# Kernel optimization log

Measured on AMD Instinct MI355X. Metric: run time of the kernel, lower is better.

## Reference

```python
import jax, jax.numpy as jnp
import numpy as np

B, S, IN, H, E, OUT = 64, 2048, 256, 512, 256, 32000


def setup_inputs() -> dict:
    key = jax.random.key(0)
    ks = jax.random.split(key, 20)
    g = lambda k, shp, fan_in: jax.random.normal(k, shp, jnp.float32) / jnp.sqrt(jnp.float32(fan_in))
    return {
        "x": jax.random.normal(ks[0], (B, IN), jnp.float32),
        "hidden": jax.random.normal(ks[1], (B, H), jnp.float32),
        "encoder_outputs": jax.random.normal(ks[2], (B, S, H), jnp.float32),
        # attention params
        "W1_w": g(ks[3], (H, E), H), "W1_b": jnp.zeros((E,), jnp.float32),
        "W2_w": g(ks[4], (H, E), H),
        "v_w": g(ks[5], (E, 1), E),
        # GRU gate params (input to gates is concat(x, context): IN+H)
        "Wxr_w": g(ks[6], (IN + H, H), IN + H), "Wxr_b": jnp.zeros((H,), jnp.float32),
        "Whr_w": g(ks[7], (H, H), H),
        "Wxz_w": g(ks[8], (IN + H, H), IN + H), "Wxz_b": jnp.zeros((H,), jnp.float32),
        "Whz_w": g(ks[9], (H, H), H),
        "Wxh_w": g(ks[10], (IN + H, H), IN + H), "Wxh_b": jnp.zeros((H,), jnp.float32),
        "Whh_w": g(ks[11], (H, H), H),
        # output projection
        "Who_w": g(ks[12], (H, OUT), H), "Who_b": jnp.zeros((OUT,), jnp.float32),
    }


def reference(x, hidden, encoder_outputs,
              W1_w, W1_b, W2_w, v_w,
              Wxr_w, Wxr_b, Whr_w,
              Wxz_w, Wxz_b, Whz_w,
              Wxh_w, Wxh_b, Whh_w,
              Who_w, Who_b):
    # Bahdanau attention
    # energy: [B, S, E]
    energy = jnp.tanh(jnp.einsum("bsh,he->bse", encoder_outputs, W1_w) + W1_b
                      + (hidden @ W2_w)[:, None, :])
    scores = jnp.einsum("bse,eo->bs", energy, v_w)          # [B, S]
    attn_weights = jax.nn.softmax(scores, axis=1)            # [B, S]
    context = jnp.einsum("bs,bsh->bh", attn_weights, encoder_outputs)  # [B, H]

    x_context = jnp.concatenate([x, context], axis=-1)       # [B, IN+H]
    reset_gate = jax.nn.sigmoid(x_context @ Wxr_w + Wxr_b + hidden @ Whr_w)
    update_gate = jax.nn.sigmoid(x_context @ Wxz_w + Wxz_b + hidden @ Whz_w)
    h_tilde = jnp.tanh(x_context @ Wxh_w + Wxh_b + (reset_gate * hidden) @ Whh_w)
    new_hidden = update_gate * hidden + (1.0 - update_gate) * h_tilde
    output = new_hidden @ Who_w + Who_b                      # [B, OUT]
    return (output, new_hidden, attn_weights)
```

## Files before the change

### kernel.cpp

```cpp
#include <hip/hip_runtime.h>

#define BB 64
#define SS 2048
#define INDIM 256
#define HH 512
#define EE 256
#define OUTD 32000

typedef __attribute__((ext_vector_type(8))) short short8;
typedef __attribute__((ext_vector_type(4))) float floatx4;

#define LOG2E 1.4426950408889634f

__device__ __forceinline__ unsigned short f2bf(float f) {
  unsigned u = __float_as_uint(f);
  return (unsigned short)((u + 0x7FFFu + ((u >> 16) & 1u)) >> 16);
}
__device__ __forceinline__ unsigned pk2(float a, float b) {
  return (unsigned)f2bf(a) | ((unsigned)f2bf(b) << 16);
}
__device__ __forceinline__ float bf2f(unsigned short u) {
  return __uint_as_float((unsigned)u << 16);
}
__device__ __forceinline__ float fast_tanh(float x) {
  float e = __builtin_amdgcn_exp2f(x * 2.8853900817779268f);
  return 1.0f - 2.0f * __builtin_amdgcn_rcpf(e + 1.0f);
}
__device__ __forceinline__ float fast_sigmoid(float x) {
  float e = __builtin_amdgcn_exp2f(-x * LOG2E);
  return __builtin_amdgcn_rcpf(1.0f + e);
}

typedef __attribute__((address_space(1))) const void g1void;
typedef __attribute__((address_space(3))) void l3void;
__device__ __forceinline__ void dma16(const void* g, void* l) {
  __builtin_amdgcn_global_load_lds((g1void*)g, (l3void*)l, 16, 0, 0);
}

#define WS_W1T   0
#define WS_HBP   262144
#define WS_CTX   786432
#define WS_NHBF  917504
#define WS_GP    1245184
#define WS_NP    6488064
#define WS_CTXP  9109504
#define WS_SUMP  25886720
#define WS_ENCB  25894912

__global__ __launch_bounds__(256) void k_pre(
    const float* __restrict__ enc, unsigned short* __restrict__ encb,
    const float* __restrict__ W1, unsigned short* __restrict__ W1t,
    const float* __restrict__ hidden, const float* __restrict__ W2,
    const float* __restrict__ W1b, float* __restrict__ hbp) {
  int blk = blockIdx.x, tid = threadIdx.x;
  if (blk < 4096) {
    int r_loc = tid >> 3, c0 = tid & 7;
    int row = blk * 32 + r_loc;
    int rs = row & 7;
    const float* src = enc + (size_t)row * HH;
    unsigned short* dst = encb + (size_t)row * HH;
#pragma unroll
    for (int k = 0; k < 8; ++k) {
      int c = c0 + k * 8;
      float4 f0 = *(const float4*)(src + c * 8);
      float4 f1 = *(const float4*)(src + c * 8 + 4);
      uint4 w;
      w.x = pk2(f0.x, f0.y); w.y = pk2(f0.z, f0.w);
      w.z = pk2(f1.x, f1.y); w.w = pk2(f1.z, f1.w);
      *(uint4*)(dst + (c ^ rs) * 8) = w;
    }
  } else if (blk < 4608) {
    int idx = (blk - 4096) * 256 + tid;
    int k = idx >> 8, e = idx & 255;
    W1t[e * HH + k] = f2bf(W1[idx]);
  } else {
    int u = blk - 4608;
    int b0 = (u & 15) * 4, seg = u >> 4, e = tid;
    int h0 = seg * 64;
    float a0 = 0, a1 = 0, a2 = 0, a3 = 0;
    if (seg == 0) { a0 = a1 = a2 = a3 = W1b[e]; }
#pragma unroll 16
    for (int h = 0; h < 64; ++h) {
      float w = W2[(h0 + h) * EE + e];
      a0 += hidden[(b0 + 0) * HH + h0 + h] * w;
      a1 += hidden[(b0 + 1) * HH + h0 + h] * w;
      a2 += hidden[(b0 + 2) * HH + h0 + h] * w;
      a3 += hidden[(b0 + 3) * HH + h0 + h] * w;
    }
    float* o = hbp + (size_t)seg * BB * EE;
    o[(b0 + 0) * EE + e] = a0; o[(b0 + 1) * EE + e] = a1;
    o[(b0 + 2) * EE + e] = a2; o[(b0 + 3) * EE + e] = a3;
  }
}

__global__ __launch_bounds__(256, 2) void k_scores(
    const unsigned short* __restrict__ encb, const unsigned short* __restrict__ W1t,
    const float* __restrict__ hbp, const float* __restrict__ vw,
    float* __restrict__ attn, float* __restrict__ ctxp, float* __restrict__ sump) {
  __shared__ unsigned short Afull[64 * 512];
  __shared__ float hb_s[EE], v_s[EE];
  __shared__ float red[4 * 64];
  __shared__ float wbuf[64];

  int tid = threadIdx.x;
  int m0 = blockIdx.x * 64;
  int b = blockIdx.x >> 5;
  int sloc = (blockIdx.x & 31) * 64;
  int lane = tid & 63, wn = tid >> 6;
  int l15 = lane & 15, quad = lane >> 4;

#pragma unroll
  for (int rr = 0; rr < 16; ++rr) {
    int r = wn * 16 + rr;
    dma16(encb + (size_t)(m0 + r) * HH + lane * 8, Afull + r * HH);
  }
  {
    float hbv = 0.0f;
#pragma unroll
    for (int s = 0; s < 8; ++s) hbv += hbp[s * BB * EE + b * EE + tid];
    hb_s[tid] = hbv;
    v_s[tid] = vw[tid];
  }
  __syncthreads();

  floatx4 acc[4][4];
#pragma unroll
  for (int i = 0; i < 4; ++i)
#pragma unroll
    for (int j = 0; j < 4; ++j) acc[i][j] = (floatx4)0.0f;

  const unsigned short* bbase = W1t + (size_t)(wn * 64) * HH;
#pragma unroll
  for (int kb = 0; kb < 16; ++kb) {
    short8 a[4];
#pragma unroll
    for (int i = 0; i < 4; ++i) {
      int r = i * 16 + l15;
      int pc = (kb * 4 + quad) ^ (l15 & 7);
      a[i] = *(const short8*)(Afull + r * HH + pc * 8);
    }
#pragma unroll
    for (int j = 0; j < 4; ++j) {
      short8 bfr = *(const short8*)(bbase + (size_t)(j * 16 + l15) * HH + kb * 32 + quad * 8);
#pragma unroll
      for (int i = 0; i < 4; ++i)
        acc[i][j] = __builtin_amdgcn_mfma_f32_16x16x32_bf16(a[i], bfr, acc[i][j], 0, 0, 0);
    }
  }
  __syncthreads();

#pragma unroll
  for (int i = 0; i < 4; ++i)
#pragma unroll
    for (int r = 0; r < 4; ++r) {
      float s = 0.0f;
#pragma unroll
      for (int j = 0; j < 4; ++j) {
        int e = wn * 64 + j * 16 + l15;
        s += fast_tanh(acc[i][j][r] + hb_s[e]) * v_s[e];
      }
#pragma unroll
      for (int off = 1; off < 16; off <<= 1) s += __shfl_xor(s, off, 64);
      if (l15 == 0) red[wn * 64 + i * 16 + quad * 4 + r] = s;
    }
  __syncthreads();
  if (tid < 64) {
    float sc = red[tid] + red[64 + tid] + red[128 + tid] + red[192 + tid];
    float e = __builtin_amdgcn_exp2f(sc * LOG2E);
    wbuf[tid] = e;
    attn[b * SS + sloc + tid] = e;
    float s = e;
#pragma unroll
    for (int off = 1; off < 64; off <<= 1) s += __shfl_xor(s, off, 64);
    if (tid == 0) sump[blockIdx.x] = s;
  }
  __syncthreads();

  float cacc[8];
#pragma unroll
  for (int j = 0; j < 8; ++j) cacc[j] = 0.0f;
#pragma unroll
  for (int rr = 0; rr < 16; ++rr) {
    int r = wn * 16 + rr;
    float w = wbuf[r];
    int pc = lane ^ (r & 7);
    short8 av = *(const short8*)(Afull + r * HH + pc * 8);
#pragma unroll
    for (int j = 0; j < 8; ++j) cacc[j] += w * bf2f((unsigned short)av[j]);
  }
  float4 c0, c1;
  c0.x = cacc[0]; c0.y = cacc[1]; c0.z = cacc[2]; c0.w = cacc[3];
  c1.x = cacc[4]; c1.y = cacc[5]; c1.z = cacc[6]; c1.w = cacc[7];
  float* cp = ctxp + ((size_t)blockIdx.x * 4 + wn) * HH + lane * 8;
  *(float4*)cp = c0;
  *(float4*)(cp + 4) = c1;
}

__global__ __launch_bounds__(256) void k_norm(float* __restrict__ attn,
                                              const float* __restrict__ ctxp,
                                              const float* __restrict__ sump,
                                              float* __restrict__ ctx) {
  int b = blockIdx.x >> 1, half = blockIdx.x & 1, tid = threadIdx.x;
  float s = 0.0f;
#pragma unroll
  for (int t = 0; t < 32; ++t) s += sump[b * 32 + t];
  float inv = 1.0f / s;
  int h = half * 256 + tid;
  float c = 0.0f;
#pragma unroll 16
  for (int t = 0; t < 128; ++t) c += ctxp[(size_t)(b * 128 + t) * HH + h];
  ctx[b * HH + h] = c * inv;
#pragma unroll
  for (int i = 0; i < 4; ++i) attn[b * SS + half * 1024 + i * 256 + tid] *= inv;
}

__device__ __forceinline__ void part_seg(
    const float* __restrict__ Wx, const float* __restrict__ Wh,
    const float* __restrict__ x, const float* __restrict__ ctx,
    const float* __restrict__ hv, int seg, int b0, int h,
    float* __restrict__ outp) {
  const float* wseg;
  const float* a0; const float* a1; const float* a2; const float* a3;
  int vk0 = seg * 64;
  if (seg < 4) {
    wseg = Wx + (size_t)vk0 * HH;
    a0 = x + (b0 + 0) * INDIM + vk0;       a1 = x + (b0 + 1) * INDIM + vk0;
    a2 = x + (b0 + 2) * INDIM + vk0;       a3 = x + (b0 + 3) * INDIM + vk0;
  } else if (seg < 12) {
    wseg = Wx + (size_t)vk0 * HH;
    int off = vk0 - 256;
    a0 = ctx + (b0 + 0) * HH + off;        a1 = ctx + (b0 + 1) * HH + off;
    a2 = ctx + (b0 + 2) * HH + off;        a3 = ctx + (b0 + 3) * HH + off;
  } else {
    int off = vk0 - 768;
    wseg = Wh + (size_t)off * HH;
    a0 = hv + (b0 + 0) * HH + off;         a1 = hv + (b0 + 1) * HH + off;
    a2 = hv + (b0 + 2) * HH + off;         a3 = hv + (b0 + 3) * HH + off;
  }
  float s0 = 0, s1 = 0, s2 = 0, s3 = 0;
#pragma unroll 16
  for (int i = 0; i < 64; ++i) {
    float w = wseg[i * HH + h];
    s0 += a0[i] * w; s1 += a1[i] * w;
    s2 += a2[i] * w; s3 += a3[i] * w;
  }
  outp[(b0 + 0) * HH + h] = s0; outp[(b0 + 1) * HH + h] = s1;
  outp[(b0 + 2) * HH + h] = s2; outp[(b0 + 3) * HH + h] = s3;
}

__global__ __launch_bounds__(512) void k_gpart(
    const float* __restrict__ x, const float* __restrict__ ctx,
    const float* __restrict__ hidden,
    const float* __restrict__ Wxr, const float* __restrict__ Whr,
    const float* __restrict__ Wxz, const float* __restrict__ Whz,
    float* __restrict__ gp) {
  int b0 = blockIdx.x * 4, seg = blockIdx.y, sel = blockIdx.z, h = threadIdx.x;
  const float* Wx = sel ? Wxz : Wxr;
  const float* Wh = sel ? Whz : Whr;
  float* outp = gp + (size_t)(sel * 20 + seg) * BB * HH;
  part_seg(Wx, Wh, x, ctx, hidden, seg, b0, h, outp);
}

__global__ __launch_bounds__(512) void k_npart(
    const float* __restrict__ x, const float* __restrict__ ctx,
    const float* __restrict__ hidden, const float* __restrict__ gp,
    const float* __restrict__ Wxrb,
    const float* __restrict__ Wxh, const float* __restrict__ Whh,
    float* __restrict__ np) {
  __shared__ float rh_s[256];
  int b0 = blockIdx.x * 4, seg = blockIdx.y, h = threadIdx.x;
  int vk0 = seg * 64;
  const float* wseg;
  const float* a0; const float* a1; const float* a2; const float* a3;
  if (seg >= 12) {
    int off = vk0 - 768;
    if (h < 256) {
      int bb = h >> 6, k = off + (h & 63);
      float r = Wxrb[k];
#pragma unroll
      for (int s = 0; s < 20; ++s) r += gp[((size_t)s * BB + b0 + bb) * HH + k];
      rh_s[h] = fast_sigmoid(r) * hidden[(b0 + bb) * HH + k];
    }
    __syncthreads();
    wseg = Whh + (size_t)off * HH;
    a0 = rh_s; a1 = rh_s + 64; a2 = rh_s + 128; a3 = rh_s + 192;
  } else if (seg < 4) {
    wseg = Wxh + (size_t)vk0 * HH;
    a0 = x + (b0 + 0) * INDIM + vk0;       a1 = x + (b0 + 1) * INDIM + vk0;
    a2 = x + (b0 + 2) * INDIM + vk0;       a3 = x + (b0 + 3) * INDIM + vk0;
  } else {
    int off = vk0 - 256;
    wseg = Wxh + (size_t)vk0 * HH;
    a0 = ctx + (b0 + 0) * HH + off;        a1 = ctx + (b0 + 1) * HH + off;
    a2 = ctx + (b0 + 2) * HH + off;        a3 = ctx + (b0 + 3) * HH + off;
  }
  float s0 = 0, s1 = 0, s2 = 0, s3 = 0;
#pragma unroll 16
  for (int i = 0; i < 64; ++i) {
    float w = wseg[i * HH + h];
    s0 += a0[i] * w; s1 += a1[i] * w;
    s2 += a2[i] * w; s3 += a3[i] * w;
  }
  float* outp = np + (size_t)seg * BB * HH;
  outp[(b0 + 0) * HH + h] = s0; outp[(b0 + 1) * HH + h] = s1;
  outp[(b0 + 2) * HH + h] = s2; outp[(b0 + 3) * HH + h] = s3;
}

__global__ __launch_bounds__(256) void k_nred(
    const float* __restrict__ np, const float* __restrict__ gp,
    const float* __restrict__ Wxzb, const float* __restrict__ Wxhb,
    const float* __restrict__ hidden,
    float* __restrict__ nh, unsigned short* __restrict__ nhbf) {
  int b = blockIdx.x >> 1, h = (blockIdx.x & 1) * 256 + threadIdx.x;
  float z = Wxzb[h];
#pragma unroll
  for (int s = 0; s < 20; ++s) z += gp[((size_t)(20 + s) * BB + b) * HH + h];
  z = fast_sigmoid(z);
  float a = Wxhb[h];
#pragma unroll
  for (int s = 0; s < 20; ++s) a += np[((size_t)s * BB + b) * HH + h];
  float ht = fast_tanh(a);
  float val = z * hidden[b * HH + h] + (1.0f - z) * ht;
  nh[b * HH + h] = val;
  nhbf[b * HH + h] = f2bf(val);
}

__global__ __launch_bounds__(256) void k_out2(const unsigned short* __restrict__ nhbf,
                                              const float* __restrict__ Who,
                                              const float* __restrict__ Whob,
                                              float* __restrict__ out) {
  int tid = threadIdx.x;
  int lane = tid & 63, w = tid >> 6;
  int l15 = lane & 15, quad = lane >> 4;
  int n = blockIdx.x * 64 + w * 16 + l15;

  floatx4 acc[4];
#pragma unroll
  for (int i = 0; i < 4; ++i) acc[i] = (floatx4)0.0f;

#pragma unroll
  for (int kc = 0; kc < 16; ++kc) {
    int k0 = kc * 32;
    float bf[8];
    const float* bp = Who + (size_t)(k0 + quad * 8) * OUTD + n;
#pragma unroll
    for (int j = 0; j < 8; ++j) bf[j] = bp[(size_t)j * OUTD];
    union { unsigned u[4]; short8 v; } bu;
#pragma unroll
    for (int j = 0; j < 4; ++j) bu.u[j] = pk2(bf[2 * j], bf[2 * j + 1]);
#pragma unroll
    for (int i = 0; i < 4; ++i) {
      short8 af = *(const short8*)(nhbf + (i * 16 + l15) * HH + k0 + quad * 8);
      acc[i] = __builtin_amdgcn_mfma_f32_16x16x32_bf16(af, bu.v, acc[i], 0, 0, 0);
    }
  }
  float bias = Whob[n];
#pragma unroll
  for (int i = 0; i < 4; ++i)
#pragma unroll
    for (int r = 0; r < 4; ++r) {
      int m = i * 16 + quad * 4 + r;
      out[(size_t)m * OUTD + n] = acc[i][r] + bias;
    }
}

extern "C" void kernel_launch(void* const* d_in, const int* in_sizes, int n_in,
                              void* d_out, int out_size, void* d_ws, size_t ws_size,
                              hipStream_t stream) {
  const float* x    = (const float*)d_in[0];
  const float* hid  = (const float*)d_in[1];
  const float* enc  = (const float*)d_in[2];
  const float* W1w  = (const float*)d_in[3];
  const float* W1b  = (const float*)d_in[4];
  const float* W2w  = (const float*)d_in[5];
  const float* vw   = (const float*)d_in[6];
  const float* Wxr  = (const float*)d_in[7];
  const float* Wxrb = (const float*)d_in[8];
  const float* Whr  = (const float*)d_in[9];
  const float* Wxz  = (const float*)d_in[10];
  const float* Wxzb = (const float*)d_in[11];
  const float* Whz  = (const float*)d_in[12];
  const float* Wxh  = (const float*)d_in[13];
  const float* Wxhb = (const float*)d_in[14];
  const float* Whh  = (const float*)d_in[15];
  const float* Who  = (const float*)d_in[16];
  const float* Whob = (const float*)d_in[17];

  float* out  = (float*)d_out;
  float* nh   = out + (size_t)BB * OUTD;
  float* attn = nh + (size_t)BB * HH;

  char* ws = (char*)d_ws;
  unsigned short* W1t  = (unsigned short*)(ws + WS_W1T);
  float* hbp  = (float*)(ws + WS_HBP);
  float* ctx  = (float*)(ws + WS_CTX);
  unsigned short* nhbf = (unsigned short*)(ws + WS_NHBF);
  float* gp   = (float*)(ws + WS_GP);
  float* np   = (float*)(ws + WS_NP);
  float* ctxp = (float*)(ws + WS_CTXP);
  float* sump = (float*)(ws + WS_SUMP);
  unsigned short* encb = (unsigned short*)(ws + WS_ENCB);

  k_pre<<<4736, 256, 0, stream>>>(enc, encb, W1w, W1t, hid, W2w, W1b, hbp);
  k_scores<<<(BB * SS) / 64, 256, 0, stream>>>(encb, W1t, hbp, vw, attn, ctxp, sump);
  k_norm<<<128, 256, 0, stream>>>(attn, ctxp, sump, ctx);
  k_gpart<<<dim3(16, 20, 2), 512, 0, stream>>>(x, ctx, hid, Wxr, Whr, Wxz, Whz, gp);
  k_npart<<<dim3(16, 20), 512, 0, stream>>>(x, ctx, hid, gp, Wxrb, Wxh, Whh, np);
  k_nred<<<128, 256, 0, stream>>>(np, gp, Wxzb, Wxhb, hid, nh, nhbf);
  k_out2<<<500, 256, 0, stream>>>(nhbf, Who, Whob, out);
}
```

Baseline: 585.1 us.

## Fuse encoder bf16 conversion into score kernel with register-prefetched K pipeline

Removes the separate pass that converts encoder_outputs to swizzled bf16 in workspace. The scores kernel now reads fp32 encoder rows directly, converts them in registers and writes them into a padded LDS tile one K-slice at a time. Global reads are prefetched three slices ahead and B fragments one slice ahead, with a barrier per slice. This drops the 128 MB bf16 write and re-read, at the cost of a per-iteration barrier, higher register pressure, and dropping the two-blocks-per-CU launch bound.

```diff
diff --git a/kernel.cpp b/kernel.cpp
--- a/kernel.cpp
+++ b/kernel.cpp
@@ -29,12 +29,6 @@
 __device__ __forceinline__ float fast_sigmoid(float x) {
   float e = __builtin_amdgcn_exp2f(-x * LOG2E);
   return __builtin_amdgcn_rcpf(1.0f + e);
-}
-
-typedef __attribute__((address_space(1))) const void g1void;
-typedef __attribute__((address_space(3))) void l3void;
-__device__ __forceinline__ void dma16(const void* g, void* l) {
-  __builtin_amdgcn_global_load_lds((g1void*)g, (l3void*)l, 16, 0, 0);
 }
 
 #define WS_W1T   0
@@ -45,36 +39,18 @@
 #define WS_NP    6488064
 #define WS_CTXP  9109504
 #define WS_SUMP  25886720
-#define WS_ENCB  25894912
 
 __global__ __launch_bounds__(256) void k_pre(
-    const float* __restrict__ enc, unsigned short* __restrict__ encb,
     const float* __restrict__ W1, unsigned short* __restrict__ W1t,
     const float* __restrict__ hidden, const float* __restrict__ W2,
     const float* __restrict__ W1b, float* __restrict__ hbp) {
   int blk = blockIdx.x, tid = threadIdx.x;
-  if (blk < 4096) {
-    int r_loc = tid >> 3, c0 = tid & 7;
-    int row = blk * 32 + r_loc;
-    int rs = row & 7;
-    const float* src = enc + (size_t)row * HH;
-    unsigned short* dst = encb + (size_t)row * HH;
-#pragma unroll
-    for (int k = 0; k < 8; ++k) {
-      int c = c0 + k * 8;
-      float4 f0 = *(const float4*)(src + c * 8);
-      float4 f1 = *(const float4*)(src + c * 8 + 4);
-      uint4 w;
-      w.x = pk2(f0.x, f0.y); w.y = pk2(f0.z, f0.w);
-      w.z = pk2(f1.x, f1.y); w.w = pk2(f1.z, f1.w);
-      *(uint4*)(dst + (c ^ rs) * 8) = w;
-    }
-  } else if (blk < 4608) {
-    int idx = (blk - 4096) * 256 + tid;
+  if (blk < 512) {
+    int idx = blk * 256 + tid;
     int k = idx >> 8, e = idx & 255;
     W1t[e * HH + k] = f2bf(W1[idx]);
   } else {
-    int u = blk - 4608;
+    int u = blk - 512;
     int b0 = (u & 15) * 4, seg = u >> 4, e = tid;
     int h0 = seg * 64;
     float a0 = 0, a1 = 0, a2 = 0, a3 = 0;
@@ -93,11 +69,12 @@
   }
 }
 
-__global__ __launch_bounds__(256, 2) void k_scores(
-    const unsigned short* __restrict__ encb, const unsigned short* __restrict__ W1t,
+#define LDA 520
+__global__ __launch_bounds__(256) void k_scores(
+    const float* __restrict__ enc, const unsigned short* __restrict__ W1t,
     const float* __restrict__ hbp, const float* __restrict__ vw,
     float* __restrict__ attn, float* __restrict__ ctxp, float* __restrict__ sump) {
-  __shared__ unsigned short Afull[64 * 512];
+  __shared__ unsigned short Afull[64 * LDA];
   __shared__ float hb_s[EE], v_s[EE];
   __shared__ float red[4 * 64];
   __shared__ float wbuf[64];
@@ -106,14 +83,6 @@
   int m0 = blockIdx.x * 64;
   int b = blockIdx.x >> 5;
   int sloc = (blockIdx.x & 31) * 64;
-  int lane = tid & 63, wn = tid >> 6;
-  int l15 = lane & 15, quad = lane >> 4;
-
-#pragma unroll
-  for (int rr = 0; rr < 16; ++rr) {
-    int r = wn * 16 + rr;
-    dma16(encb + (size_t)(m0 + r) * HH + lane * 8, Afull + r * HH);
-  }
   {
     float hbv = 0.0f;
 #pragma unroll
@@ -121,7 +90,13 @@
     hb_s[tid] = hbv;
     v_s[tid] = vw[tid];
   }
-  __syncthreads();
+
+  int lane = tid & 63, wn = tid >> 6;
+  int l15 = lane & 15, quad = lane >> 4;
+
+  int row0 = tid >> 3, kg = tid & 7;
+  const float* base0 = enc + (size_t)(m0 + row0) * HH + kg * 4;
+  const float* base1 = enc + (size_t)(m0 + 32 + row0) * HH + kg * 4;
 
   floatx4 acc[4][4];
 #pragma unroll
@@ -129,22 +104,55 @@
 #pragma unroll
     for (int j = 0; j < 4; ++j) acc[i][j] = (floatx4)0.0f;
 
-  const unsigned short* bbase = W1t + (size_t)(wn * 64) * HH;
+  float4 pf0[3], pf1[3];
+#pragma unroll
+  for (int d = 0; d < 3; ++d) {
+    pf0[d] = *(const float4*)(base0 + d * 32);
+    pf1[d] = *(const float4*)(base1 + d * 32);
+  }
+
+  short8 bcur[4];
+#pragma unroll
+  for (int j = 0; j < 4; ++j)
+    bcur[j] = *(const short8*)(W1t + (wn * 64 + j * 16 + l15) * HH + quad * 8);
+
 #pragma unroll
   for (int kb = 0; kb < 16; ++kb) {
+    int slot = kb % 3;
+    {
+      float4 f = pf0[slot];
+      uint2 w; w.x = pk2(f.x, f.y); w.y = pk2(f.z, f.w);
+      *(uint2*)(Afull + row0 * LDA + kb * 32 + kg * 4) = w;
+      f = pf1[slot];
+      uint2 w2; w2.x = pk2(f.x, f.y); w2.y = pk2(f.z, f.w);
+      *(uint2*)(Afull + (row0 + 32) * LDA + kb * 32 + kg * 4) = w2;
+    }
+    if (kb + 3 < 16) {
+      pf0[slot] = *(const float4*)(base0 + (kb + 3) * 32);
+      pf1[slot] = *(const float4*)(base1 + (kb + 3) * 32);
+    }
+    short8 bnx[4];
+    if (kb + 1 < 16) {
+      int kkn = (kb + 1) * 32 + quad * 8;
+#pragma unroll
+      for (int j = 0; j < 4; ++j)
+        bnx[j] = *(const short8*)(W1t + (wn * 64 + j * 16 + l15) * HH + kkn);
+    }
+    asm volatile("s_waitcnt lgkmcnt(0)" ::: "memory");
+    __builtin_amdgcn_s_barrier();
+    int kk = kb * 32 + quad * 8;
     short8 a[4];
 #pragma unroll
-    for (int i = 0; i < 4; ++i) {
-      int r = i * 16 + l15;
-      int pc = (kb * 4 + quad) ^ (l15 & 7);
-      a[i] = *(const short8*)(Afull + r * HH + pc * 8);
-    }
-#pragma unroll
-    for (int j = 0; j < 4; ++j) {
-      short8 bfr = *(const short8*)(bbase + (size_t)(j * 16 + l15) * HH + kb * 32 + quad * 8);
+    for (int i = 0; i < 4; ++i)
+      a[i] = *(const short8*)(Afull + (i * 16 + l15) * LDA + kk);
+#pragma unroll
+    for (int j = 0; j < 4; ++j)
 #pragma unroll
       for (int i = 0; i < 4; ++i)
-        acc[i][j] = __builtin_amdgcn_mfma_f32_16x16x32_bf16(a[i], bfr, acc[i][j], 0, 0, 0);
+        acc[i][j] = __builtin_amdgcn_mfma_f32_16x16x32_bf16(a[i], bcur[j], acc[i][j], 0, 0, 0);
+    if (kb + 1 < 16) {
+#pragma unroll
+      for (int j = 0; j < 4; ++j) bcur[j] = bnx[j];
     }
   }
   __syncthreads();
@@ -183,8 +191,7 @@
   for (int rr = 0; rr < 16; ++rr) {
     int r = wn * 16 + rr;
     float w = wbuf[r];
-    int pc = lane ^ (r & 7);
-    short8 av = *(const short8*)(Afull + r * HH + pc * 8);
+    short8 av = *(const short8*)(Afull + r * LDA + lane * 8);
 #pragma unroll
     for (int j = 0; j < 8; ++j) cacc[j] += w * bf2f((unsigned short)av[j]);
   }
@@ -399,10 +406,9 @@
   float* np   = (float*)(ws + WS_NP);
   float* ctxp = (float*)(ws + WS_CTXP);
   float* sump = (float*)(ws + WS_SUMP);
-  unsigned short* encb = (unsigned short*)(ws + WS_ENCB);
-
-  k_pre<<<4736, 256, 0, stream>>>(enc, encb, W1w, W1t, hid, W2w, W1b, hbp);
-  k_scores<<<(BB * SS) / 64, 256, 0, stream>>>(encb, W1t, hbp, vw, attn, ctxp, sump);
+
+  k_pre<<<640, 256, 0, stream>>>(W1w, W1t, hid, W2w, W1b, hbp);
+  k_scores<<<(BB * SS) / 64, 256, 0, stream>>>(enc, W1t, hbp, vw, attn, ctxp, sump);
   k_norm<<<128, 256, 0, stream>>>(attn, ctxp, sump, ctx);
   k_gpart<<<dim3(16, 20, 2), 512, 0, stream>>>(x, ctx, hid, Wxr, Whr, Wxz, Whz, gp);
   k_npart<<<dim3(16, 20), 512, 0, stream>>>(x, ctx, hid, gp, Wxrb, Wxh, Whh, np);
```

After: 508.8 us. 1.15x faster.
